# Kernel tuning notes

Measured on AMD Instinct MI355X. Metric: run time of the kernel, lower is better.

The kernel has to match this reference:

```python
import jax, jax.numpy as jnp
import numpy as np
from jax import lax

DEPTH, HEADS, DH, DIM, M, V, NUM_EMB, D_VQ = 6, 8, 64, 512, 256, 523, 512, 64


def _ln(x, g, b):
    mu = jnp.mean(x, -1, keepdims=True)
    var = jnp.var(x, -1, keepdims=True)
    return (x - mu) * lax.rsqrt(var + 1e-5) * g + b


def _softmax_kernel(data, proj, is_query):
    # FAVOR+ positive softmax features (performer-pytorch softmax_kernel)
    dn = data * (data.shape[-1] ** -0.25)
    dd = jnp.einsum('bhld,md->bhlm', dn, proj)
    diag = 0.5 * jnp.sum(dn * dn, axis=-1, keepdims=True)
    mx = jnp.max(dd, axis=-1, keepdims=True) if is_query else jnp.max(dd)
    return jnp.exp(dd - diag - lax.stop_gradient(mx)) * (proj.shape[0] ** -0.5) + 1e-4


def _causal_linear_attn(qp, kp, v):
    # out_t = qp_t . cumsum_t(kp v^T) / (qp_t . cumsum_t(kp))
    kc = jnp.cumsum(kp, axis=2)
    den = jnp.einsum('bhlm,bhlm->bhl', qp, kc)
    kv = jnp.cumsum(jnp.einsum('bhlm,bhld->bhlmd', kp, v), axis=2)
    return jnp.einsum('bhlm,bhlmd->bhld', qp, kv) / den[..., None]


def _vq_encode(_x, conv1_w, conv1_b, conv2_w, conv2_b, codebook):
    dn = ('NCDHW', 'OIDHW', 'NCDHW')
    h = lax.conv_general_dilated(_x, conv1_w, (2, 2, 2), [(1, 1)] * 3, dimension_numbers=dn)
    h = jax.nn.relu(h + conv1_b[None, :, None, None, None])
    h = lax.conv_general_dilated(h, conv2_w, (2, 2, 2), [(1, 1)] * 3, dimension_numbers=dn)
    h = h + conv2_b[None, :, None, None, None]                 # [N, D, 4,4,4]
    z = jnp.transpose(h, (0, 2, 3, 4, 1))                      # [N, 4,4,4, D]
    flat = z.reshape(-1, z.shape[-1])
    d2 = (jnp.sum(flat * flat, 1, keepdims=True)
          - 2.0 * flat @ codebook.T
          + jnp.sum(codebook * codebook, 1)[None, :])
    inds = jnp.argmin(d2, axis=1).astype(jnp.int32)
    return inds.reshape(z.shape[:4])                           # [N, 4,4,4]


def _performer_loss(seq, tok_emb, pos_emb, proj, ln1_g, ln1_b, wq, wk, wv, wo, bo,
                    ln2_g, ln2_b, ff1_w, ff1_b, ff2_w, ff2_b, lnf_g, lnf_b,
                    logits_w, logits_b):
    inp, tgt = seq[:, :-1], seq[:, 1:]
    b, L = inp.shape
    h = tok_emb[inp] + pos_emb[:L][None]
    split = lambda t: jnp.transpose(t.reshape(b, L, HEADS, DH), (0, 2, 1, 3))
    for l in range(DEPTH):
        x1 = _ln(h, ln1_g[l], ln1_b[l])
        q, k, v = split(x1 @ wq[l]), split(x1 @ wk[l]), split(x1 @ wv[l])
        qp = _softmax_kernel(q, proj[l], True)
        kp = _softmax_kernel(k, proj[l], False)
        o = _causal_linear_attn(qp, kp, v)
        o = jnp.transpose(o, (0, 2, 1, 3)).reshape(b, L, DIM)
        h = h + o @ wo[l] + bo[l]
        x2 = _ln(h, ln2_g[l], ln2_b[l])
        h = h + jax.nn.gelu(x2 @ ff1_w[l] + ff1_b[l]) @ ff2_w[l] + ff2_b[l]
    h = _ln(h, lnf_g, lnf_b)
    logits = h @ logits_w + logits_b
    lp = jax.nn.log_softmax(logits, axis=-1)
    nll = -jnp.take_along_axis(lp, tgt[..., None], axis=-1)[..., 0]
    return jnp.mean(nll)


def setup_inputs() -> dict:
    key = jax.random.key(0)
    ks = jax.random.split(key, 24)
    n = lambda k, sh, s=0.02: (jax.random.normal(k, sh) * s).astype(jnp.float32)
    bs = 16
    return {
        'x': jax.random.normal(ks[0], (bs, 1, 16, 16, 16), jnp.float32),
        'xn': jax.random.normal(ks[1], (bs, 1, 1, 16, 16, 16), jnp.float32),
        'i': jax.random.randint(ks[2], (bs, 3), 0, V, jnp.int32),
        # frozen VQ-VAE
        'conv1_w': n(ks[3], (32, 1, 4, 4, 4), 0.1), 'conv1_b': jnp.zeros((32,), jnp.float32),
        'conv2_w': n(ks[4], (D_VQ, 32, 4, 4, 4), 0.05), 'conv2_b': jnp.zeros((D_VQ,), jnp.float32),
        'codebook': jax.random.normal(ks[5], (NUM_EMB, D_VQ), jnp.float32),
        # FAVOR+ random-feature projections (non-trainable buffer)
        'proj': jax.random.normal(ks[6], (DEPTH, M, DH), jnp.float32),
        # performer params
        'tok_emb': n(ks[7], (V, DIM)), 'pos_emb': n(ks[8], (131, DIM)),
        'ln1_g': jnp.ones((DEPTH, DIM), jnp.float32), 'ln1_b': jnp.zeros((DEPTH, DIM), jnp.float32),
        'wq': n(ks[9], (DEPTH, DIM, DIM)), 'wk': n(ks[10], (DEPTH, DIM, DIM)),
        'wv': n(ks[11], (DEPTH, DIM, DIM)), 'wo': n(ks[12], (DEPTH, DIM, DIM)),
        'bo': jnp.zeros((DEPTH, DIM), jnp.float32),
        'ln2_g': jnp.ones((DEPTH, DIM), jnp.float32), 'ln2_b': jnp.zeros((DEPTH, DIM), jnp.float32),
        'ff1_w': n(ks[13], (DEPTH, DIM, 4 * DIM)), 'ff1_b': jnp.zeros((DEPTH, 4 * DIM), jnp.float32),
        'ff2_w': n(ks[14], (DEPTH, 4 * DIM, DIM)), 'ff2_b': jnp.zeros((DEPTH, DIM), jnp.float32),
        'lnf_g': jnp.ones((DIM,), jnp.float32), 'lnf_b': jnp.zeros((DIM,), jnp.float32),
        'logits_w': n(ks[15], (DIM, V)), 'logits_b': jnp.zeros((V,), jnp.float32),
    }


def reference(x, xn, i, conv1_w, conv1_b, conv2_w, conv2_b, codebook, proj,
              tok_emb, pos_emb, ln1_g, ln1_b, wq, wk, wv, wo, bo, ln2_g, ln2_b,
              ff1_w, ff1_b, ff2_w, ff2_b, lnf_g, lnf_b, logits_w, logits_b):
    bs = x.shape[0]
    _xn = xn.reshape((-1,) + xn.shape[2:])            # (b n) c x y z
    _x = jnp.concatenate([x, _xn], axis=0)
    inds = _vq_encode(_x, conv1_w, conv1_b, conv2_w, conv2_b, codebook)
    inds_i = inds[:bs].reshape(bs, -1)                # b (x y z)
    inds_r = inds[bs:].reshape(bs, -1)                # b (n x y z)
    seq = jnp.concatenate([i.astype(jnp.int32), inds_r, inds_i], axis=1)  # [b, 131]
    return _performer_loss(seq, tok_emb, pos_emb, proj, ln1_g, ln1_b, wq, wk, wv, wo,
                           bo, ln2_g, ln2_b, ff1_w, ff1_b, ff2_w, ff2_b,
                           lnf_g, lnf_b, logits_w, logits_b)
```

## Files before the change

### kernel.cpp

```cpp
#include <hip/hip_runtime.h>

#define SEQL 130
#define LSEQ 131
#define DIMM 512
#define NHEADS 8
#define MF 256
#define VSZ 523
#define NROWS (16*SEQL)
#define NBH (16*NHEADS)
#define NBHL (NBH*SEQL)
#define QSEG 1064960
#define WLAYER 3145728

typedef __attribute__((ext_vector_type(8))) short short8;
typedef __attribute__((ext_vector_type(8))) unsigned short us8;
typedef __attribute__((ext_vector_type(4))) unsigned short us4;
typedef __attribute__((ext_vector_type(4))) float f32x4;

__device__ __forceinline__ unsigned short f2bf(float f){
  unsigned int u = __float_as_uint(f);
  u += 0x7fffu + ((u>>16)&1u);
  return (unsigned short)(u>>16);
}
__device__ __forceinline__ float bf2f(unsigned short h){
  return __uint_as_float(((unsigned int)h)<<16);
}
__device__ __forceinline__ float gelu_f(float x){
  float x3 = x*x*x;
  return 0.5f*x*(1.f+tanhf(0.7978845608028654f*(x+0.044715f*x3)));
}
__device__ __forceinline__ unsigned enc_max(float f){
  unsigned u = __float_as_uint(f);
  return (u & 0x80000000u) ? ~u : (u | 0x80000000u);
}
__device__ __forceinline__ float dec_max(unsigned k){
  unsigned u = (k>>31) ? (k & 0x7fffffffu) : ~k;
  return __uint_as_float(u);
}
__device__ __forceinline__ void gload16(const void* g, void* lds){
  __builtin_amdgcn_global_load_lds(
      (const __attribute__((address_space(1))) void*)g,
      (__attribute__((address_space(3))) void*)lds, 16, 0, 0);
}
__device__ __forceinline__ float blk_sum(float v){
  #pragma unroll
  for(int off=32;off;off>>=1) v += __shfl_xor(v,off);
  __shared__ float tmp_s[4];
  int t=threadIdx.x;
  if((t&63)==0) tmp_s[t>>6]=v;
  __syncthreads();
  v = tmp_s[0]+tmp_s[1]+tmp_s[2]+tmp_s[3];
  __syncthreads();
  return v;
}
__device__ __forceinline__ float blk_max(float v){
  #pragma unroll
  for(int off=32;off;off>>=1) v = fmaxf(v,__shfl_xor(v,off));
  __shared__ float tmp_m[4];
  int t=threadIdx.x;
  if((t&63)==0) tmp_m[t>>6]=v;
  __syncthreads();
  v = fmaxf(fmaxf(tmp_m[0],tmp_m[1]),fmaxf(tmp_m[2],tmp_m[3]));
  __syncthreads();
  return v;
}
__device__ __forceinline__ int tok_at(const int* __restrict__ iarr,
    const int* __restrict__ inds, int b, int p){
  if(p<3)  return iarr[b*3+p];
  if(p<67) return inds[(16+b)*64 + (p-3)];
  return inds[b*64 + (p-67)];
}

__global__ __launch_bounds__(256) void conv1_k(const float* __restrict__ x,
    const float* __restrict__ xn, const float* __restrict__ w,
    const float* __restrict__ bias, float* __restrict__ out){
  int idx = blockIdx.x*256 + threadIdx.x;
  if(idx >= 32*32*8*8*8) return;
  int ow = idx & 7, oh = (idx>>3)&7, od = (idx>>6)&7, oc = (idx>>9)&31, n = idx>>14;
  const float* xp = (n<16) ? (x + n*4096) : (xn + (n-16)*4096);
  const float* wp = w + oc*64;
  float acc = bias[oc];
  #pragma unroll
  for(int kd=0;kd<4;kd++){ int id = od*2-1+kd; if((unsigned)id>=16u) continue;
    #pragma unroll
    for(int kh=0;kh<4;kh++){ int ih = oh*2-1+kh; if((unsigned)ih>=16u) continue;
      #pragma unroll
      for(int kw=0;kw<4;kw++){ int iw = ow*2-1+kw; if((unsigned)iw>=16u) continue;
        acc += xp[(id*16+ih)*16+iw]*wp[(kd*4+kh)*4+kw];
      }}}
  out[idx] = fmaxf(acc,0.f);
}

__global__ __launch_bounds__(256) void im2col_k(const float* __restrict__ c1,
    unsigned short* __restrict__ icol){
  int tid = blockIdx.x*256 + threadIdx.x;
  size_t e0 = (size_t)tid*8;
  int r = (int)(e0 >> 11);
  int k0 = (int)(e0 & 2047);
  int n = r>>6, od = (r>>4)&3, oh = (r>>2)&3, ow = r&3;
  int ic = k0>>6, kd = (k0>>4)&3, kh0 = (k0>>2)&3;
  int id = od*2 - 1 + kd;
  us8 u = {};
  if((unsigned)id < 8u){
    const float* base = c1 + (size_t)(n*32+ic)*512 + id*64;
    #pragma unroll
    for(int j=0;j<8;j++){
      int kh = kh0 + (j>>2), kw = j&3;
      int ih = oh*2 - 1 + kh, iw = ow*2 - 1 + kw;
      float v = 0.f;
      if((unsigned)ih < 8u && (unsigned)iw < 8u) v = base[ih*8 + iw];
      u[j] = f2bf(v);
    }
  }
  *(us8*)(icol + e0) = u;
}

__global__ __launch_bounds__(256) void vq_k(const float* __restrict__ z,
    const float* __restrict__ cb, int* __restrict__ inds){
  int nf = blockIdx.x;
  __shared__ float zs[64];
  int t = threadIdx.x;
  if(t<64) zs[t] = z[(size_t)nf*64 + t];
  __syncthreads();
  float best = 3.0e38f; int bi = 0;
  for(int j=t; j<512; j+=256){
    const float* cr = cb + j*64;
    float dot=0.f, nn=0.f;
    #pragma unroll 8
    for(int d=0;d<64;d++){ float cv=cr[d]; dot += zs[d]*cv; nn += cv*cv; }
    float dist = nn - 2.f*dot;
    if(dist < best){ best=dist; bi=j; }
  }
  #pragma unroll
  for(int off=32;off;off>>=1){
    float ob = __shfl_down(best,off); int oi = __shfl_down(bi,off);
    if(ob<best || (ob==best && oi<bi)){ best=ob; bi=oi; }
  }
  __shared__ float rb[4]; __shared__ int ri[4];
  if((t&63)==0){ rb[t>>6]=best; ri[t>>6]=bi; }
  __syncthreads();
  if(t==0){
    for(int wv=1;wv<4;wv++){ if(rb[wv]<best || (rb[wv]==best && ri[wv]<bi)){ best=rb[wv]; bi=ri[wv]; } }
    inds[nf]=bi;
  }
}

__global__ __launch_bounds__(256) void embed_k(const int* __restrict__ iarr,
    const int* __restrict__ inds, const float* __restrict__ tok,
    const float* __restrict__ pos, float* __restrict__ h){
  int idx = blockIdx.x*256 + threadIdx.x;
  int c = idx & 511; int row = idx >> 9;
  int b = row/SEQL, l = row - b*SEQL;
  int tk = tok_at(iarr, inds, b, l);
  h[idx] = tok[tk*DIMM + c] + pos[l*DIMM + c];
}

__global__ __launch_bounds__(256) void ln_k(const float* __restrict__ in,
    const float* __restrict__ g, const float* __restrict__ bb,
    unsigned short* __restrict__ out){
  int w = threadIdx.x>>6, l = threadIdx.x&63;
  int row = blockIdx.x*4 + w;
  const float* xr = in + (size_t)row*DIMM + l*8;
  f32x4 v0 = *(const f32x4*)xr;
  f32x4 v1 = *(const f32x4*)(xr+4);
  float s = v0[0]+v0[1]+v0[2]+v0[3]+v1[0]+v1[1]+v1[2]+v1[3];
  float ss = v0[0]*v0[0]+v0[1]*v0[1]+v0[2]*v0[2]+v0[3]*v0[3]
           + v1[0]*v1[0]+v1[1]*v1[1]+v1[2]*v1[2]+v1[3]*v1[3];
  #pragma unroll
  for(int off=32;off;off>>=1){ s += __shfl_xor(s,off); ss += __shfl_xor(ss,off); }
  float mu = s*(1.f/512.f);
  float var = ss*(1.f/512.f) - mu*mu;
  float inv = rsqrtf(var + 1e-5f);
  const float* gp = g + l*8; const float* bp = bb + l*8;
  us8 u;
  #pragma unroll
  for(int j=0;j<4;j++){
    u[j]   = f2bf((v0[j]-mu)*inv*gp[j]   + bp[j]);
    u[4+j] = f2bf((v1[j]-mu)*inv*gp[4+j] + bp[4+j]);
  }
  *(us8*)(out + (size_t)row*DIMM + l*8) = u;
}

__global__ __launch_bounds__(256) void prep_k(const float* __restrict__ wq,
    const float* __restrict__ wk, const float* __restrict__ wv,
    const float* __restrict__ wo, const float* __restrict__ ff1,
    const float* __restrict__ ff2, unsigned short* __restrict__ wall,
    const float* __restrict__ conv2_w, unsigned short* __restrict__ cw2b,
    const float* __restrict__ proj, unsigned short* __restrict__ projb,
    const float* __restrict__ logits_w, unsigned short* __restrict__ logt,
    unsigned int* __restrict__ gmaxbits){
  int bid0 = blockIdx.x;
  int t = threadIdx.x;
  if(bid0==0 && t<8) gmaxbits[t] = 0u;
  if(bid0 < 18432){
    int lyr = bid0 / 3072;
    int bid = bid0 - lyr*3072;
    unsigned short* wl = wall + (size_t)lyr*WLAYER;
    const float* src; unsigned short* dst;
    int n0, k0, srcN, dstK;
    if(bid < 768){
      int nt = bid % 48, kt = bid / 48;
      n0 = nt*32; k0 = kt*32;
      int seg = n0 >> 9;
      src = (seg==0 ? wq : seg==1 ? wk : wv) + (size_t)lyr*262144;
      dst = wl; srcN = 512; dstK = 512;
    } else if(bid < 1024){
      int b2 = bid-768; int nt = b2 % 16, kt = b2 / 16;
      n0 = nt*32; k0 = kt*32; src = wo + (size_t)lyr*262144;
      dst = wl + 786432; srcN = 512; dstK = 512;
    } else if(bid < 2048){
      int b2 = bid-1024; int nt = b2 % 64, kt = b2 / 64;
      n0 = nt*32; k0 = kt*32; src = ff1 + (size_t)lyr*1048576;
      dst = wl + 1048576; srcN = 2048; dstK = 512;
    } else {
      int b2 = bid-2048; int nt = b2 % 16, kt = b2 / 16;
      n0 = nt*32; k0 = kt*32; src = ff2 + (size_t)lyr*1048576;
      dst = wl + 2097152; srcN = 512; dstK = 2048;
    }
    int srcCol0 = (bid < 768) ? (n0 & 0x1ff) : n0;
    __shared__ float tile[32][33];
    int c = t&31, r = t>>5;
    #pragma unroll
    for(int j=0;j<4;j++)
      tile[r+8*j][c] = src[(size_t)(k0+r+8*j)*srcN + srcCol0 + c];
    __syncthreads();
    #pragma unroll
    for(int j=0;j<4;j++){
      int n = n0 + r + 8*j;
      dst[(size_t)n*dstK + k0 + c] = f2bf(tile[c][r+8*j]);
    }
    return;
  }
  if(bid0 < 18544){
    const float* src; unsigned short* dst; int i;
    if(bid0 < 18496){ i = (bid0-18432)*256 + t; src = conv2_w; dst = cw2b; }
    else            { i = (bid0-18496)*256 + t; src = proj;    dst = projb; }
    const float* s = src + (size_t)i*8;
    us8 u;
    #pragma unroll
    for(int j=0;j<8;j++) u[j] = f2bf(s[j]);
    *(us8*)(dst + (size_t)i*8) = u;
    return;
  }
  {
    int b2 = bid0 - 18544;
    int nt = b2 % 17, kt = b2 / 17;
    int n0 = nt*32, k0 = kt*32;
    __shared__ float tile[32][33];
    int c = t&31, r = t>>5;
    #pragma unroll
    for(int j=0;j<4;j++){
      int n = n0+c;
      tile[r+8*j][c] = (n<VSZ) ? logits_w[(size_t)(k0+r+8*j)*VSZ + n] : 0.f;
    }
    __syncthreads();
    #pragma unroll
    for(int j=0;j<4;j++){
      int n = n0 + r + 8*j;
      if(n<VSZ) logt[(size_t)n*512 + k0 + c] = f2bf(tile[c][r+8*j]);
    }
  }
}

template<int MODE>
__global__ __launch_bounds__(256) void gemm64x128_k(const unsigned short* __restrict__ A,
    const unsigned short* __restrict__ Bt, const float* __restrict__ bias,
    unsigned short* __restrict__ Cb, int M, int N, int K){
  __shared__ __attribute__((aligned(16))) unsigned short As[2][4096];
  __shared__ __attribute__((aligned(16))) unsigned short Bs[2][8192];
  int t = threadIdx.x, w = t>>6, l = t&63;
  const int m0 = blockIdx.y*64, n0 = blockIdx.x*128;
  int wr = w>>1, wc = w&1;
  f32x4 acc[2][4] = {};
  auto stage = [&](unsigned short* Ad, unsigned short* Bd, int k0){
    #pragma unroll
    for(int i=0;i<2;i++){
      int c = w*2 + i;
      int r = c*8 + (l>>3);
      int gc = k0 + (((l&7) ^ (r&7))<<3);
      int ar = m0 + r; if(ar >= M) ar = 0;
      gload16(A + (size_t)ar*K + gc, Ad + c*512);
    }
    #pragma unroll
    for(int i=0;i<4;i++){
      int c = w*4 + i;
      int r = c*8 + (l>>3);
      int gc = k0 + (((l&7) ^ (r&7))<<3);
      gload16(Bt + (size_t)(n0+r)*K + gc, Bd + c*512);
    }
  };
  stage(As[0], Bs[0], 0);
  int NTk = K>>6, buf = 0;
  for(int kt=0; kt<NTk; kt++){
    __syncthreads();
    if(kt+1 < NTk) stage(As[buf^1], Bs[buf^1], (kt+1)*64);
    const unsigned short* Ab = &As[buf][0];
    const unsigned short* Bb = &Bs[buf][0];
    #pragma unroll
    for(int kk=0;kk<2;kk++){
      short8 af[2], bf[4];
      #pragma unroll
      for(int m=0;m<2;m++){
        int row = wr*32 + m*16 + (l&15);
        int slot = kk*4 + (l>>4);
        af[m] = *(const short8*)(Ab + row*64 + ((slot^(row&7))<<3));
      }
      #pragma unroll
      for(int n=0;n<4;n++){
        int col = wc*64 + n*16 + (l&15);
        int slot = kk*4 + (l>>4);
        bf[n] = *(const short8*)(Bb + col*64 + ((slot^(col&7))<<3));
      }
      #pragma unroll
      for(int m=0;m<2;m++)
        #pragma unroll
        for(int n=0;n<4;n++)
          acc[m][n] = __builtin_amdgcn_mfma_f32_16x16x32_bf16(af[m], bf[n], acc[m][n], 0, 0, 0);
    }
    buf ^= 1;
  }
  #pragma unroll
  for(int m=0;m<2;m++){
    #pragma unroll
    for(int n=0;n<4;n++){
      int col = n0 + wc*64 + n*16 + (l&15);
      #pragma unroll
      for(int i=0;i<4;i++){
        int row = m0 + wr*32 + m*16 + (l>>4)*4 + i;
        if(row < M){
          float v = acc[m][n][i];
          if(MODE==1){
            v *= (col < 1024) ? 0.35355339059327378f : 1.0f;
            int seg = col>>9, d0 = col&511;
            int hh = d0>>6, d = d0&63;
            int bb = row/SEQL, ll = row - bb*SEQL;
            Cb[(size_t)seg*QSEG + (((size_t)(bb*NHEADS+hh))*SEQL + ll)*64 + d] = f2bf(v);
          } else {
            v += bias[col];
            v = gelu_f(v);
            Cb[(size_t)row*N+col] = f2bf(v);
          }
        }
      }
    }
  }
}

template<int MODE>
__global__ __launch_bounds__(256) void mgemm_k(const unsigned short* __restrict__ A,
    const unsigned short* __restrict__ Bt, const float* __restrict__ bias,
    float* __restrict__ Cf, int M, int N, int K){
  __shared__ __attribute__((aligned(16))) unsigned short As[2][4096];
  __shared__ __attribute__((aligned(16))) unsigned short Bs[2][4096];
  int t = threadIdx.x;
  const int m0 = blockIdx.y*64, n0 = blockIdx.x*64;
  int w = t>>6, l = t&63;
  int wr = w>>1, wc = w&1;
  f32x4 acc[2][2] = {};
  auto stage = [&](unsigned short* Ad, unsigned short* Bd, int k0){
    #pragma unroll
    for(int i=0;i<2;i++){
      int c = w*2 + i;
      int r = c*8 + (l>>3);
      int gc = k0 + (((l&7) ^ (r&7))<<3);
      int ar = m0 + r; if(ar >= M) ar = 0;
      gload16(A + (size_t)ar*K + gc, Ad + c*512);
      int br = n0 + r; if(br >= N) br = 0;
      gload16(Bt + (size_t)br*K + gc, Bd + c*512);
    }
  };
  stage(As[0], Bs[0], 0);
  int NT = K>>6;
  int buf = 0;
  for(int kt=0; kt<NT; kt++){
    __syncthreads();
    if(kt+1 < NT) stage(As[buf^1], Bs[buf^1], (kt+1)*64);
    const unsigned short* Ab = &As[buf][0];
    const unsigned short* Bb = &Bs[buf][0];
    #pragma unroll
    for(int kk=0;kk<2;kk++){
      short8 af[2], bf[2];
      #pragma unroll
      for(int m=0;m<2;m++){
        int row = wr*32 + m*16 + (l&15);
        int slot = kk*4 + (l>>4);
        af[m] = *(const short8*)(Ab + row*64 + ((slot^(row&7))<<3));
      }
      #pragma unroll
      for(int n=0;n<2;n++){
        int col = wc*32 + n*16 + (l&15);
        int slot = kk*4 + (l>>4);
        bf[n] = *(const short8*)(Bb + col*64 + ((slot^(col&7))<<3));
      }
      #pragma unroll
      for(int m=0;m<2;m++)
        #pragma unroll
        for(int n=0;n<2;n++)
          acc[m][n] = __builtin_amdgcn_mfma_f32_16x16x32_bf16(af[m], bf[n], acc[m][n], 0, 0, 0);
    }
    buf ^= 1;
  }
  #pragma unroll
  for(int m=0;m<2;m++){
    #pragma unroll
    for(int n=0;n<2;n++){
      int col = n0 + wc*32 + n*16 + (l&15);
      #pragma unroll
      for(int i=0;i<4;i++){
        int row = m0 + wr*32 + m*16 + (l>>4)*4 + i;
        if(row < M && col < N){
          if(MODE==3) Cf[(size_t)row*N+col] += acc[m][n][i] + bias[col];
          else        Cf[(size_t)row*N+col]  = acc[m][n][i] + bias[col];
        }
      }
    }
  }
}

template<int ACC>
__global__ __launch_bounds__(256) void mgemm32_k(const unsigned short* __restrict__ A,
    const unsigned short* __restrict__ Bt, const float* __restrict__ bias,
    float* __restrict__ Cf, int N, int K){
  __shared__ __attribute__((aligned(16))) unsigned short As[2][2048];
  __shared__ __attribute__((aligned(16))) unsigned short Bs[2][4096];
  int t = threadIdx.x;
  const int m0 = blockIdx.y*32, n0 = blockIdx.x*64;
  int w = t>>6, l = t&63;
  int wm = w&1, wn2 = w>>1;
  f32x4 acc[2] = {};
  auto stage = [&](unsigned short* Ad, unsigned short* Bd, int k0){
    {
      int c = w;
      int r = c*8 + (l>>3);
      int gc = k0 + (((l&7) ^ (r&7))<<3);
      gload16(A + (size_t)(m0+r)*K + gc, Ad + c*512);
    }
    #pragma unroll
    for(int i=0;i<2;i++){
      int c = w*2 + i;
      int r = c*8 + (l>>3);
      int gc = k0 + (((l&7) ^ (r&7))<<3);
      gload16(Bt + (size_t)(n0+r)*K + gc, Bd + c*512);
    }
  };
  stage(As[0], Bs[0], 0);
  int NT = K>>6;
  int buf = 0;
  for(int kt=0; kt<NT; kt++){
    __syncthreads();
    if(kt+1 < NT) stage(As[buf^1], Bs[buf^1], (kt+1)*64);
    const unsigned short* Ab = &As[buf][0];
    const unsigned short* Bb = &Bs[buf][0];
    #pragma unroll
    for(int kk=0;kk<2;kk++){
      int arow = wm*16 + (l&15);
      int slot = kk*4 + (l>>4);
      short8 af = *(const short8*)(Ab + arow*64 + ((slot^(arow&7))<<3));
      #pragma unroll
      for(int n=0;n<2;n++){
        int col = (wn2*2+n)*16 + (l&15);
        short8 bf = *(const short8*)(Bb + col*64 + ((slot^(col&7))<<3));
        acc[n] = __builtin_amdgcn_mfma_f32_16x16x32_bf16(af, bf, acc[n], 0, 0, 0);
      }
    }
    buf ^= 1;
  }
  #pragma unroll
  for(int n=0;n<2;n++){
    int col = n0 + (wn2*2+n)*16 + (l&15);
    float bv = bias[col];
    #pragma unroll
    for(int i=0;i<4;i++){
      int row = m0 + wm*16 + (l>>4)*4 + i;
      if(ACC) Cf[(size_t)row*N+col] += acc[n][i] + bv;
      else    Cf[(size_t)row*N+col]  = acc[n][i] + bv;
    }
  }
}

__global__ __launch_bounds__(256) void featA_k(const unsigned short* __restrict__ qn,
    const unsigned short* __restrict__ kn, const unsigned short* __restrict__ projl,
    unsigned short* __restrict__ qp, unsigned int* __restrict__ gmaxbits){
  int z = blockIdx.y;
  const unsigned short* dn = z ? kn : qn;
  __shared__ __attribute__((aligned(16))) float uni[32*264];
  __shared__ __attribute__((aligned(16))) unsigned short dns[2048];
  unsigned short* ps = (unsigned short*)uni;
  int t = threadIdx.x;
  int w = t>>6, l = t&63;
  size_t R0 = (size_t)blockIdx.x*32;
  {
    int c = w; int r = c*8 + (l>>3);
    int gc = (((l&7) ^ (r&7))<<3);
    gload16(dn + (R0+r)*64 + gc, dns + c*512);
  }
  #pragma unroll
  for(int i=0;i<8;i++){
    int c = w*8 + i; int r = c*8 + (l>>3);
    int gc = (((l&7) ^ (r&7))<<3);
    gload16(projl + (size_t)r*64 + gc, ps + c*512);
  }
  __syncthreads();
  int rt = w&1, cb = (w>>1)*8;
  f32x4 acc[8] = {};
  #pragma unroll
  for(int kk=0;kk<2;kk++){
    int ar = rt*16 + (l&15);
    int slot = kk*4 + (l>>4);
    short8 a = *(const short8*)(dns + ar*64 + ((slot^(ar&7))<<3));
    #pragma unroll
    for(int ct=0;ct<8;ct++){
      int br = (cb+ct)*16 + (l&15);
      short8 b = *(const short8*)(ps + br*64 + ((slot^(br&7))<<3));
      acc[ct] = __builtin_amdgcn_mfma_f32_16x16x32_bf16(a, b, acc[ct], 0, 0, 0);
    }
  }
  __syncthreads();
  #pragma unroll
  for(int ct=0;ct<8;ct++){
    int col = (cb+ct)*16 + (l&15);
    #pragma unroll
    for(int i=0;i<4;i++){
      int row = rt*16 + (l>>4)*4 + i;
      uni[row*264 + col] = acc[ct][i];
    }
  }
  __syncthreads();
  int r = t>>3, sub = t&7;
  float* rowp = uni + r*264 + sub*32;
  f32x4 v[8];
  #pragma unroll
  for(int jj=0;jj<8;jj++) v[jj] = *(const f32x4*)(rowp + jj*4);
  float m = -3.0e38f;
  #pragma unroll
  for(int jj=0;jj<8;jj++)
    #pragma unroll
    for(int i=0;i<4;i++) m = fmaxf(m, v[jj][i]);
  m = fmaxf(m, __shfl_xor(m,1));
  m = fmaxf(m, __shfl_xor(m,2));
  m = fmaxf(m, __shfl_xor(m,4));
  if(z==0){
    us8 dvu = *(const us8*)(dns + r*64 + ((sub^(r&7))<<3));
    float s2 = 0.f;
    #pragma unroll
    for(int j=0;j<8;j++){ float xx = bf2f(dvu[j]); s2 += xx*xx; }
    s2 += __shfl_xor(s2,1); s2 += __shfl_xor(s2,2); s2 += __shfl_xor(s2,4);
    float ds = 0.5f*s2;
    unsigned short* op = qp + (R0+r)*256 + sub*32;
    #pragma unroll
    for(int jj=0;jj<8;jj++){
      us4 u4;
      #pragma unroll
      for(int i=0;i<4;i++) u4[i] = f2bf(expf(v[jj][i] - ds - m)*0.0625f + 1e-4f);
      *(us4*)(op + jj*4) = u4;
    }
  } else {
    float bm = m;
    bm = fmaxf(bm, __shfl_xor(bm,8));
    bm = fmaxf(bm, __shfl_xor(bm,16));
    bm = fmaxf(bm, __shfl_xor(bm,32));
    __shared__ float wm[4];
    if(l==0) wm[w] = bm;
    __syncthreads();
    if(t==0){
      float g = fmaxf(fmaxf(wm[0],wm[1]),fmaxf(wm[2],wm[3]));
      atomicMax(gmaxbits, enc_max(g));
    }
  }
}

__global__ __launch_bounds__(256) void featB_k(const unsigned short* __restrict__ kn,
    const unsigned short* __restrict__ projl, const unsigned int* __restrict__ gmaxbits,
    unsigned short* __restrict__ kp){
  __shared__ __attribute__((aligned(16))) float uni[32*264];
  __shared__ __attribute__((aligned(16))) unsigned short dns[2048];
  unsigned short* ps = (unsigned short*)uni;
  int t = threadIdx.x;
  int w = t>>6, l = t&63;
  size_t R0 = (size_t)blockIdx.x*32;
  {
    int c = w; int r = c*8 + (l>>3);
    int gc = (((l&7) ^ (r&7))<<3);
    gload16(kn + (R0+r)*64 + gc, dns + c*512);
  }
  #pragma unroll
  for(int i=0;i<8;i++){
    int c = w*8 + i; int r = c*8 + (l>>3);
    int gc = (((l&7) ^ (r&7))<<3);
    gload16(projl + (size_t)r*64 + gc, ps + c*512);
  }
  __syncthreads();
  int rt = w&1, cb = (w>>1)*8;
  f32x4 acc[8] = {};
  #pragma unroll
  for(int kk=0;kk<2;kk++){
    int ar = rt*16 + (l&15);
    int slot = kk*4 + (l>>4);
    short8 a = *(const short8*)(dns + ar*64 + ((slot^(ar&7))<<3));
    #pragma unroll
    for(int ct=0;ct<8;ct++){
      int br = (cb+ct)*16 + (l&15);
      short8 b = *(const short8*)(ps + br*64 + ((slot^(br&7))<<3));
      acc[ct] = __builtin_amdgcn_mfma_f32_16x16x32_bf16(a, b, acc[ct], 0, 0, 0);
    }
  }
  __syncthreads();
  #pragma unroll
  for(int ct=0;ct<8;ct++){
    int col = (cb+ct)*16 + (l&15);
    #pragma unroll
    for(int i=0;i<4;i++){
      int row = rt*16 + (l>>4)*4 + i;
      uni[row*264 + col] = acc[ct][i];
    }
  }
  __syncthreads();
  float g = dec_max(gmaxbits[0]);
  int r = t>>3, sub = t&7;
  us8 dvu = *(const us8*)(dns + r*64 + ((sub^(r&7))<<3));
  float s2 = 0.f;
  #pragma unroll
  for(int j=0;j<8;j++){ float xx = bf2f(dvu[j]); s2 += xx*xx; }
  s2 += __shfl_xor(s2,1); s2 += __shfl_xor(s2,2); s2 += __shfl_xor(s2,4);
  float ds = 0.5f*s2;
  float* rowp = uni + r*264 + sub*32;
  unsigned short* op = kp + (R0+r)*256 + sub*32;
  #pragma unroll
  for(int jj=0;jj<8;jj++){
    f32x4 v = *(const f32x4*)(rowp + jj*4);
    us4 u4;
    #pragma unroll
    for(int i=0;i<4;i++) u4[i] = f2bf(expf(v[i] - ds - g)*0.0625f + 1e-4f);
    *(us4*)(op + jj*4) = u4;
  }
}

__global__ __launch_bounds__(256) void attn_k(const unsigned short* __restrict__ qp,
    const unsigned short* __restrict__ kp, const unsigned short* __restrict__ vn,
    unsigned short* __restrict__ ob){
  int qt = blockIdx.x, bh = blockIdx.y;
  int b = bh>>3, hh = bh&7;
  __shared__ __attribute__((aligned(16))) unsigned short qs[8192];
  __shared__ __attribute__((aligned(16))) unsigned short ks[5*8192];
  __shared__ __attribute__((aligned(16))) unsigned short VTs[5*2176];
  __shared__ __attribute__((aligned(16))) unsigned short Sb[5*1152];
  __shared__ float dens[2][32];
  int t = threadIdx.x;
  int w = t>>6, l = t&63;
  int qh = w>>1, nc = w&1;
  #pragma unroll
  for(int i=0;i<4;i++){
    int c = w*4 + i; int r = (c<<1) + (l>>5); int sl = l&31;
    int gc = ((sl ^ (r&7))<<3);
    int gr = qt*32 + r; if(gr >= SEQL) gr = 0;
    gload16(qp + ((size_t)bh*SEQL + gr)*256 + gc, qs + c*512);
  }
  for(int kt=0; kt<=qt; kt++){
    #pragma unroll
    for(int i=0;i<4;i++){
      int c = w*4 + i; int r = (c<<1) + (l>>5); int sl = l&31;
      int gc = ((sl ^ (r&7))<<3);
      int gk = kt*32 + r; if(gk >= SEQL) gk = 0;
      gload16(kp + ((size_t)bh*SEQL + gk)*256 + gc, ks + kt*8192 + c*512);
    }
    {
      int rr = t>>3, od = (t&7)*8;
      int gk = kt*32 + rr;
      us8 uv = {};
      if(gk < SEQL) uv = *(const us8*)(vn + ((size_t)bh*SEQL + gk)*64 + od);
      #pragma unroll
      for(int j=0;j<8;j++) VTs[kt*2176 + (od+j)*34 + rr] = uv[j];
    }
  }
  __syncthreads();
  float dreg[4] = {0.f,0.f,0.f,0.f};
  for(int kt=0; kt<=qt; kt++){
    const unsigned short* kb = ks + kt*8192;
    f32x4 sacc = {};
    #pragma unroll
    for(int kk=0;kk<8;kk++){
      int ar = qh*16 + (l&15); int slot = kk*4 + (l>>4);
      short8 a = *(const short8*)(qs + ar*256 + ((slot^(ar&7))<<3));
      int br = nc*16 + (l&15);
      short8 bb2 = *(const short8*)(kb + br*256 + ((slot^(br&7))<<3));
      sacc = __builtin_amdgcn_mfma_f32_16x16x32_bf16(a, bb2, sacc, 0, 0, 0);
    }
    int scol = nc*16 + (l&15);
    int gcol = kt*32 + scol;
    float dp[4];
    #pragma unroll
    for(int i=0;i<4;i++){
      int sr = qh*16 + (l>>4)*4 + i;
      int grw = qt*32 + sr;
      float v2 = sacc[i];
      if(gcol > grw) v2 = 0.f;
      Sb[kt*1152 + sr*36 + scol] = f2bf(v2);
      dp[i] = v2;
    }
    #pragma unroll
    for(int off=1;off<16;off<<=1)
      #pragma unroll
      for(int i=0;i<4;i++) dp[i] += __shfl_xor(dp[i], off);
    #pragma unroll
    for(int i=0;i<4;i++) dreg[i] += dp[i];
  }
  if((l&15)==0){
    #pragma unroll
    for(int i=0;i<4;i++) dens[nc][qh*16 + (l>>4)*4 + i] = dreg[i];
  }
  __syncthreads();
  f32x4 oacc[2] = {};
  for(int kt=0; kt<=qt; kt++){
    short8 a2 = *(const short8*)(Sb + kt*1152 + (qh*16 + (l&15))*36 + (l>>4)*8);
    #pragma unroll
    for(int n2=0;n2<2;n2++){
      int d = nc*32 + n2*16 + (l&15);
      short8 b2 = *(const short8*)(VTs + kt*2176 + d*34 + (l>>4)*8);
      oacc[n2] = __builtin_amdgcn_mfma_f32_16x16x32_bf16(a2, b2, oacc[n2], 0, 0, 0);
    }
  }
  #pragma unroll
  for(int n2=0;n2<2;n2++){
    int d = nc*32 + n2*16 + (l&15);
    #pragma unroll
    for(int i=0;i<4;i++){
      int rit = qh*16 + (l>>4)*4 + i;
      int gr = qt*32 + rit;
      if(gr < SEQL){
        float inv = 1.f/(dens[0][rit] + dens[1][rit]);
        ob[((size_t)(b*SEQL+gr))*DIMM + hh*64 + d] = f2bf(oacc[n2][i]*inv);
      }
    }
  }
}

__global__ __launch_bounds__(256) void loss_k(const float* __restrict__ logits,
    const int* __restrict__ iarr, const int* __restrict__ inds,
    float* __restrict__ rnll){
  int row = blockIdx.x; int t = threadIdx.x;
  const float* lr = logits + (size_t)row*VSZ;
  float m = -3.0e38f;
  for(int j=t;j<VSZ;j+=256) m = fmaxf(m, lr[j]);
  m = blk_max(m);
  float s = 0.f;
  for(int j=t;j<VSZ;j+=256) s += expf(lr[j]-m);
  s = blk_sum(s);
  if(t==0){
    int b = row/SEQL, l = row - b*SEQL;
    int tgt = tok_at(iarr, inds, b, l+1);
    rnll[row] = (m + logf(s)) - lr[tgt];
  }
}

__global__ __launch_bounds__(256) void fin_k(const float* __restrict__ rnll,
    float* __restrict__ out){
  int t = threadIdx.x;
  float s = 0.f;
  for(int i=t;i<NROWS;i+=256) s += rnll[i];
  s = blk_sum(s);
  if(t==0) out[0] = s/(float)NROWS;
}

extern "C" void kernel_launch(void* const* d_in, const int* in_sizes, int n_in,
                              void* d_out, int out_size, void* d_ws, size_t ws_size,
                              hipStream_t stream){
  (void)in_sizes; (void)n_in; (void)out_size; (void)ws_size;
  const float* x        = (const float*)d_in[0];
  const float* xn       = (const float*)d_in[1];
  const int*   iarr     = (const int*)  d_in[2];
  const float* conv1_w  = (const float*)d_in[3];
  const float* conv1_b  = (const float*)d_in[4];
  const float* conv2_w  = (const float*)d_in[5];
  const float* conv2_b  = (const float*)d_in[6];
  const float* codebook = (const float*)d_in[7];
  const float* proj     = (const float*)d_in[8];
  const float* tok_emb  = (const float*)d_in[9];
  const float* pos_emb  = (const float*)d_in[10];
  const float* ln1_g    = (const float*)d_in[11];
  const float* ln1_b    = (const float*)d_in[12];
  const float* wq       = (const float*)d_in[13];
  const float* wk       = (const float*)d_in[14];
  const float* wv       = (const float*)d_in[15];
  const float* wo       = (const float*)d_in[16];
  const float* bo       = (const float*)d_in[17];
  const float* ln2_g    = (const float*)d_in[18];
  const float* ln2_b    = (const float*)d_in[19];
  const float* ff1_w    = (const float*)d_in[20];
  const float* ff1_b    = (const float*)d_in[21];
  const float* ff2_w    = (const float*)d_in[22];
  const float* ff2_b    = (const float*)d_in[23];
  const float* lnf_g    = (const float*)d_in[24];
  const float* lnf_b    = (const float*)d_in[25];
  const float* logits_w = (const float*)d_in[26];
  const float* logits_b = (const float*)d_in[27];

  float* wsf = (float*)d_ws;
  size_t off = 0;
  unsigned short* qp_bf = (unsigned short*)(wsf + off); off += 2129920;
  unsigned short* kp_bf = (unsigned short*)(wsf + off); off += 2129920;
  float* h = wsf + off; off += 1064960;
  unsigned short* x1b = (unsigned short*)(wsf + off); off += 532480;
  unsigned short* qkvb = (unsigned short*)(wsf + off); off += 1597440;
  unsigned short* ob  = (unsigned short*)(wsf + off); off += 532480;
  unsigned short* projb = (unsigned short*)(wsf + off); off += 49152;
  unsigned short* wall  = (unsigned short*)(wsf + off); off += 9437184;
  unsigned short* logt  = (unsigned short*)(wsf + off); off += 133888;
  unsigned short* ffmid = (unsigned short*)(wsf + off); off += 2129920;
  float* logits = wsf + off; off += 1087840;
  int* inds = (int*)(wsf + off); off += 2048;
  unsigned int* gmaxbits = (unsigned int*)(wsf + off); off += 64;
  float* rnll = wsf + off; off += 2112;

  float* c1 = logits;
  unsigned short* icol = ffmid;
  float* zbuf = (float*)qp_bf;
  unsigned short* cw2b = (unsigned short*)kp_bf;

  unsigned short* qnb = qkvb;
  unsigned short* knb = qkvb + QSEG;
  unsigned short* vnb = qkvb + 2*QSEG;

  prep_k<<<18816,256,0,stream>>>(wq, wk, wv, wo, ff1_w, ff2_w, wall,
      conv2_w, cw2b, proj, projb, logits_w, logt, gmaxbits);
  conv1_k<<<2048,256,0,stream>>>(x, xn, conv1_w, conv1_b, c1);
  im2col_k<<<2048,256,0,stream>>>(c1, icol);
  mgemm32_k<0><<<dim3(1,64),256,0,stream>>>(icol, cw2b, conv2_b, zbuf, 64, 2048);
  vq_k<<<2048,256,0,stream>>>(zbuf, codebook, inds);
  embed_k<<<(NROWS*DIMM)/256,256,0,stream>>>(iarr, inds, tok_emb, pos_emb, h);

  for(int l=0;l<6;l++){
    unsigned short* wl    = wall + (size_t)l*WLAYER;
    unsigned short* wqkvt = wl;
    unsigned short* wot   = wl + 786432;
    unsigned short* ff1t  = wl + 1048576;
    unsigned short* ff2t  = wl + 2097152;
    ln_k<<<520,256,0,stream>>>(h, ln1_g+l*DIMM, ln1_b+l*DIMM, x1b);
    gemm64x128_k<1><<<dim3(12,33),256,0,stream>>>(x1b, wqkvt, nullptr, qkvb, NROWS, 1536, DIMM);
    featA_k<<<dim3(520,2),256,0,stream>>>(qnb, knb, projb + l*16384, qp_bf, gmaxbits + l);
    featB_k<<<520,256,0,stream>>>(knb, projb + l*16384, gmaxbits + l, kp_bf);
    attn_k<<<dim3(5,NBH),256,0,stream>>>(qp_bf, kp_bf, vnb, ob);
    mgemm32_k<1><<<dim3(8,65),256,0,stream>>>(ob, wot, bo+l*DIMM, h, DIMM, DIMM);
    ln_k<<<520,256,0,stream>>>(h, ln2_g+l*DIMM, ln2_b+l*DIMM, x1b);
    gemm64x128_k<4><<<dim3(16,33),256,0,stream>>>(x1b, ff1t, ff1_b+l*2048, ffmid, NROWS, 2048, DIMM);
    mgemm_k<3><<<dim3(8,33),256,0,stream>>>(ffmid, ff2t, ff2_b+l*DIMM, h, NROWS, DIMM, 2048);
  }

  ln_k<<<520,256,0,stream>>>(h, lnf_g, lnf_b, x1b);
  mgemm_k<0><<<dim3(9,33),256,0,stream>>>(x1b, logt, logits_b, logits, NROWS, VSZ, DIMM);
  loss_k<<<NROWS,256,0,stream>>>(logits, iarr, inds, rnll);
  fin_k<<<1,256,0,stream>>>(rnll, (float*)d_out);
}
```

Before: 781.4 us.

## Double-buffer K/V tiles in causal attention and use 32-row GEMM for FF2

The attention kernel now keeps two buffers for the K features, V transpose and score tiles instead of holding all five tiles at once. The score and output MFMAs are fused into one loop, and the next tile's load is prefetched while the current one is computed. This cuts LDS use, which may allow more blocks per CU, and overlaps loads with math, at the cost of extra barriers per iteration. Separately, the FF2 residual GEMM switches to the 32-row-tile accumulate kernel, doubling the block count to 8x65 for better CU fill.

```diff
diff --git a/kernel.cpp b/kernel.cpp
--- a/kernel.cpp
+++ b/kernel.cpp
@@ -346,7 +346,6 @@
   }
 }
 
-template<int MODE>
 __global__ __launch_bounds__(256) void mgemm_k(const unsigned short* __restrict__ A,
     const unsigned short* __restrict__ Bt, const float* __restrict__ bias,
     float* __restrict__ Cf, int M, int N, int K){
@@ -409,8 +408,7 @@
       for(int i=0;i<4;i++){
         int row = m0 + wr*32 + m*16 + (l>>4)*4 + i;
         if(row < M && col < N){
-          if(MODE==3) Cf[(size_t)row*N+col] += acc[m][n][i] + bias[col];
-          else        Cf[(size_t)row*N+col]  = acc[m][n][i] + bias[col];
+          Cf[(size_t)row*N+col] = acc[m][n][i] + bias[col];
         }
       }
     }
@@ -641,9 +639,9 @@
   int qt = blockIdx.x, bh = blockIdx.y;
   int b = bh>>3, hh = bh&7;
   __shared__ __attribute__((aligned(16))) unsigned short qs[8192];
-  __shared__ __attribute__((aligned(16))) unsigned short ks[5*8192];
-  __shared__ __attribute__((aligned(16))) unsigned short VTs[5*2176];
-  __shared__ __attribute__((aligned(16))) unsigned short Sb[5*1152];
+  __shared__ __attribute__((aligned(16))) unsigned short ks[2][8192];
+  __shared__ __attribute__((aligned(16))) unsigned short VTs[2][2176];
+  __shared__ __attribute__((aligned(16))) unsigned short Sb[2][1152];
   __shared__ float dens[2][32];
   int t = threadIdx.x;
   int w = t>>6, l = t&63;
@@ -655,34 +653,35 @@
     int gr = qt*32 + r; if(gr >= SEQL) gr = 0;
     gload16(qp + ((size_t)bh*SEQL + gr)*256 + gc, qs + c*512);
   }
-  for(int kt=0; kt<=qt; kt++){
+  auto stageK = [&](int kt, int bu){
     #pragma unroll
     for(int i=0;i<4;i++){
       int c = w*4 + i; int r = (c<<1) + (l>>5); int sl = l&31;
       int gc = ((sl ^ (r&7))<<3);
       int gk = kt*32 + r; if(gk >= SEQL) gk = 0;
-      gload16(kp + ((size_t)bh*SEQL + gk)*256 + gc, ks + kt*8192 + c*512);
-    }
-    {
-      int rr = t>>3, od = (t&7)*8;
-      int gk = kt*32 + rr;
-      us8 uv = {};
-      if(gk < SEQL) uv = *(const us8*)(vn + ((size_t)bh*SEQL + gk)*64 + od);
-      #pragma unroll
-      for(int j=0;j<8;j++) VTs[kt*2176 + (od+j)*34 + rr] = uv[j];
-    }
-  }
-  __syncthreads();
+      gload16(kp + ((size_t)bh*SEQL + gk)*256 + gc, ks[bu] + c*512);
+    }
+    int rr = t>>3, od = (t&7)*8;
+    int gk = kt*32 + rr;
+    us8 uv = {};
+    if(gk < SEQL) uv = *(const us8*)(vn + ((size_t)bh*SEQL + gk)*64 + od);
+    #pragma unroll
+    for(int j=0;j<8;j++) VTs[bu][(od+j)*34 + rr] = uv[j];
+  };
+  stageK(0, 0);
   float dreg[4] = {0.f,0.f,0.f,0.f};
+  f32x4 oacc[2] = {};
   for(int kt=0; kt<=qt; kt++){
-    const unsigned short* kb = ks + kt*8192;
+    int cur = kt&1;
+    __syncthreads();
+    if(kt < qt) stageK(kt+1, cur^1);
     f32x4 sacc = {};
     #pragma unroll
     for(int kk=0;kk<8;kk++){
       int ar = qh*16 + (l&15); int slot = kk*4 + (l>>4);
       short8 a = *(const short8*)(qs + ar*256 + ((slot^(ar&7))<<3));
       int br = nc*16 + (l&15);
-      short8 bb2 = *(const short8*)(kb + br*256 + ((slot^(br&7))<<3));
+      short8 bb2 = *(const short8*)(ks[cur] + br*256 + ((slot^(br&7))<<3));
       sacc = __builtin_amdgcn_mfma_f32_16x16x32_bf16(a, bb2, sacc, 0, 0, 0);
     }
     int scol = nc*16 + (l&15);
@@ -694,7 +693,7 @@
       int grw = qt*32 + sr;
       float v2 = sacc[i];
       if(gcol > grw) v2 = 0.f;
-      Sb[kt*1152 + sr*36 + scol] = f2bf(v2);
+      Sb[cur][sr*36 + scol] = f2bf(v2);
       dp[i] = v2;
     }
     #pragma unroll
@@ -703,22 +702,20 @@
       for(int i=0;i<4;i++) dp[i] += __shfl_xor(dp[i], off);
     #pragma unroll
     for(int i=0;i<4;i++) dreg[i] += dp[i];
-  }
-  if((l&15)==0){
-    #pragma unroll
-    for(int i=0;i<4;i++) dens[nc][qh*16 + (l>>4)*4 + i] = dreg[i];
-  }
-  __syncthreads();
-  f32x4 oacc[2] = {};
-  for(int kt=0; kt<=qt; kt++){
-    short8 a2 = *(const short8*)(Sb + kt*1152 + (qh*16 + (l&15))*36 + (l>>4)*8);
+    __syncthreads();
+    short8 a2 = *(const short8*)(Sb[cur] + (qh*16 + (l&15))*36 + (l>>4)*8);
     #pragma unroll
     for(int n2=0;n2<2;n2++){
       int d = nc*32 + n2*16 + (l&15);
-      short8 b2 = *(const short8*)(VTs + kt*2176 + d*34 + (l>>4)*8);
+      short8 b2 = *(const short8*)(VTs[cur] + d*34 + (l>>4)*8);
       oacc[n2] = __builtin_amdgcn_mfma_f32_16x16x32_bf16(a2, b2, oacc[n2], 0, 0, 0);
     }
   }
+  if((l&15)==0){
+    #pragma unroll
+    for(int i=0;i<4;i++) dens[nc][qh*16 + (l>>4)*4 + i] = dreg[i];
+  }
+  __syncthreads();
   #pragma unroll
   for(int n2=0;n2<2;n2++){
     int d = nc*32 + n2*16 + (l&15);
@@ -842,11 +839,11 @@
     mgemm32_k<1><<<dim3(8,65),256,0,stream>>>(ob, wot, bo+l*DIMM, h, DIMM, DIMM);
     ln_k<<<520,256,0,stream>>>(h, ln2_g+l*DIMM, ln2_b+l*DIMM, x1b);
     gemm64x128_k<4><<<dim3(16,33),256,0,stream>>>(x1b, ff1t, ff1_b+l*2048, ffmid, NROWS, 2048, DIMM);
-    mgemm_k<3><<<dim3(8,33),256,0,stream>>>(ffmid, ff2t, ff2_b+l*DIMM, h, NROWS, DIMM, 2048);
+    mgemm32_k<1><<<dim3(8,65),256,0,stream>>>(ffmid, ff2t, ff2_b+l*DIMM, h, DIMM, 2048);
   }
 
   ln_k<<<520,256,0,stream>>>(h, lnf_g, lnf_b, x1b);
-  mgemm_k<0><<<dim3(9,33),256,0,stream>>>(x1b, logt, logits_b, logits, NROWS, VSZ, DIMM);
+  mgemm_k<<<dim3(9,33),256,0,stream>>>(x1b, logt, logits_b, logits, NROWS, VSZ, DIMM);
   loss_k<<<NROWS,256,0,stream>>>(logits, iarr, inds, rnll);
   fin_k<<<1,256,0,stream>>>(rnll, (float*)d_out);
 }
```

After: 731.6 us. 6.4% less time.
